# Kernel optimization log

Hardware: AMD Instinct MI355X
Metric: run time of the kernel (lower is better)

Reference implementation:

```python
import math
import jax, jax.numpy as jnp
import numpy as np

B, N, F, FE = 16, 24, 128, 128   # crystals, atoms/crystal, atom feat, edge feat
NUM_Z = 100                       # num_atomic_numbers
GAUSS_STOP, BASIS_W = 6.0, 1.0
RADIUS_RATE = 1.0
N_CONV, N_FC, FC_F = 3, 4, 128
REP = 1                           # PBC replication per axis (27 images); exact for our cells
ZDIM = 2 * F + FE


def setup_inputs() -> dict:
    key = jax.random.key(0)
    ks = jax.random.split(key, 12)
    # cubic cells with side length in [8, 10) Angstrom -> rep per axis is exactly 1
    L = 8.0 + 2.0 * jax.random.uniform(ks[0], (B,))
    cell = L[:, None, None] * jnp.eye(3, dtype=jnp.float32)          # [B,3,3]
    frac = jax.random.uniform(ks[1], (B, N, 3))
    pos = jnp.einsum('bnd,bde->bne', frac, cell).reshape(B * N, 3)   # [B*N,3]
    atomic_numbers = jax.random.randint(ks[2], (B * N,), 1, NUM_Z + 1)
    batch = jnp.repeat(jnp.arange(B), N)
    emb = jax.random.normal(ks[3], (NUM_Z, F)) * 0.1                 # embedding table
    s = 1.0 / math.sqrt(ZDIM)
    conv_Wf = jax.random.normal(ks[4], (N_CONV, ZDIM, F)) * s
    conv_bf = jnp.zeros((N_CONV, F))
    conv_Ws = jax.random.normal(ks[5], (N_CONV, ZDIM, F)) * s
    conv_bs = jnp.zeros((N_CONV, F))
    sf = 1.0 / math.sqrt(FC_F)
    fc_W = jax.random.normal(ks[6], (N_FC - 1, FC_F, FC_F)) * sf
    fc_b = jnp.zeros((N_FC - 1, FC_F))
    W_out = jax.random.normal(ks[7], (FC_F, 1)) * sf
    b_out = jnp.zeros((1,))
    return {'pos': pos, 'cell': cell, 'emb': emb,
            'conv_Wf': conv_Wf, 'conv_bf': conv_bf,
            'conv_Ws': conv_Ws, 'conv_bs': conv_bs,
            'fc_W': fc_W, 'fc_b': fc_b, 'W_out': W_out, 'b_out': b_out,
            'atomic_numbers': atomic_numbers, 'batch': batch}


def _spectral_normalize(W, iters=5, eps=1e-12):
    # power iteration; sigma differentiable through W only (u,v detached) as in torch
    u = jnp.ones((W.shape[1],), W.dtype)
    u = u / jnp.linalg.norm(u)
    for _ in range(iters):
        v = W @ u
        v = v / (jnp.linalg.norm(v) + eps)
        u = W.T @ v
        u = u / (jnp.linalg.norm(u) + eps)
    u = jax.lax.stop_gradient(u)
    v = jax.lax.stop_gradient(v)
    sigma = v @ (W @ u)
    return W / sigma


def _forward(pos, cell, emb, conv_Wf, conv_bf, conv_Ws, conv_bs,
             fc_W, fc_b, W_out, b_out, atomic_numbers):
    # ---- graph construction (PBC all-pairs, fixed 27 images, masked) ----
    r = jnp.arange(-REP, REP + 1, dtype=cell.dtype)
    grid = jnp.stack(jnp.meshgrid(r, r, r, indexing='ij'), -1).reshape(-1, 3)  # [27,3]
    pbc = jnp.einsum('cd,bde->bce', grid, cell)                                # [B,27,3]
    posb = pos.reshape(B, N, 3)
    # disp[b,i,j,c] = pos_i - (pos_j + offset_c)
    disp = posb[:, :, None, None, :] - (posb[:, None, :, None, :] + pbc[:, None, None, :, :])
    dsqr = jnp.sum(disp * disp, -1)                                            # [B,N,N,27]
    cross = jnp.cross(cell[:, 1], cell[:, 2])
    vol = jnp.sum(cell[:, 0] * cross, -1)
    radius = RADIUS_RATE * (jnp.abs(vol) / N) ** (1.0 / 3.0)                   # [B]
    rb = radius[:, None, None, None]
    mask = (dsqr <= rb * rb) & (dsqr > 1e-4)
    dist = jnp.sqrt(jnp.maximum(dsqr, 1e-12))
    mf = mask.astype(pos.dtype)
    edge_w = (jnp.cos(dist * math.pi / rb) + 1.0) * mf                         # [B,N,N,27]
    # GaussianSmearing
    goff = jnp.linspace(0.0, GAUSS_STOP, FE)
    coeff = -0.5 / (BASIS_W * (goff[1] - goff[0])) ** 2
    edge_attr = jnp.exp(coeff * (dist[..., None] - goff) ** 2)                 # [B,N,N,27,FE]

    # ---- node features ----
    feat = jnp.tanh(emb[atomic_numbers - 1]).reshape(B, N, F)

    # ---- continuous graph convs (CGCNN-style gated conv, edge_weight scaled) ----
    for l in range(N_CONV):
        Wf, Ws = conv_Wf[l], conv_Ws[l]
        gi = feat @ Wf[:F]; gj = feat @ Wf[F:2 * F]
        ge = jnp.einsum('bijce,ef->bijcf', edge_attr, Wf[2 * F:])
        g = jax.nn.sigmoid(gi[:, :, None, None, :] + gj[:, None, :, None, :] + ge + conv_bf[l])
        si = feat @ Ws[:F]; sj = feat @ Ws[F:2 * F]
        se = jnp.einsum('bijce,ef->bijcf', edge_attr, Ws[2 * F:])
        sc = jax.nn.softplus(si[:, :, None, None, :] + sj[:, None, :, None, :] + se + conv_bs[l])
        msg = g * sc * edge_w[..., None]                                       # [B,N,N,27,F]
        feat = jax.nn.softplus(feat + msg.sum((2, 3)))                         # aggregate at i

    # ---- global mean pool + spectral-norm MLP head ----
    h = feat.mean(1)                                                           # [B,F]
    for l in range(N_FC - 1):
        h = jax.nn.softplus(h @ _spectral_normalize(fc_W[l]) + fc_b[l])
    return h @ W_out + b_out                                                   # [B,1]


def reference(pos, cell, emb, conv_Wf, conv_bf, conv_Ws, conv_bs,
              fc_W, fc_b, W_out, b_out, atomic_numbers, batch):
    return _forward(pos, cell, emb, conv_Wf, conv_bf, conv_Ws, conv_bs,
                    fc_W, fc_b, W_out, b_out, atomic_numbers)
```

## Files before the change

### kernel.cpp

```cpp
#include <hip/hip_runtime.h>
#include <math.h>

#define NB 16
#define NN 24
#define NA 384
#define FF 128
#define CC 27
#define MAXNBR 32
#define MAXE 24
#define NT 20

__device__ float g_sigma[4];
__device__ float g_projA[NA*4*FF];
__device__ float g_projB[NA*4*FF];
__device__ float g_feat [NA*FF];
__device__ __align__(128) int g_flag[NA][32];
__device__ __align__(128) int g_sigdone[32];
__device__ __align__(128) int g_batchdone[32];

__device__ __forceinline__ float softplusf(float x){ return fmaxf(x,0.f) + log1pf(expf(-fabsf(x))); }
__device__ __forceinline__ float sigmoidf(float x){ return 1.f/(1.f+expf(-x)); }
__device__ __forceinline__ void st_agent(float* p, float v){
  __hip_atomic_store(p, v, __ATOMIC_RELAXED, __HIP_MEMORY_SCOPE_AGENT);
}
__device__ __forceinline__ float ld_agent(const float* p){
  return __hip_atomic_load(p, __ATOMIC_RELAXED, __HIP_MEMORY_SCOPE_AGENT);
}
__device__ __forceinline__ void st_agent_i(int* p, int v){
  __hip_atomic_store(p, v, __ATOMIC_RELAXED, __HIP_MEMORY_SCOPE_AGENT);
}
__device__ __forceinline__ int ld_agent_i(const int* p){
  return __hip_atomic_load(p, __ATOMIC_RELAXED, __HIP_MEMORY_SCOPE_AGENT);
}

__device__ __forceinline__ void band_dot2(const float* __restrict__ ga, int kmin,
                                          const float* __restrict__ Wf2,
                                          const float* __restrict__ Ws2, int f,
                                          float& ge, float& se)
{
  float g = 0.f, s = 0.f;
  #pragma unroll
  for (int t = 0; t < NT; t++) {
    float a = ga[t];
    int k = kmin + t;
    g += a * Wf2[k*FF+f];
    s += a * Ws2[k*FF+f];
  }
  ge = g; se = s;
}

__device__ __forceinline__ float gemv_q(const float* __restrict__ Wf,
                                        const float* __restrict__ Ws,
                                        const float* s_ft, int q, int f)
{
  const float* W = (q==0) ? Wf : (q==1) ? (Wf + FF*FF) : (q==2) ? Ws : (Ws + FF*FF);
  float s = 0.f;
  #pragma unroll 16
  for (int k = 0; k < FF; k++) s += s_ft[k]*W[k*FF+f];
  return s;
}

__device__ __forceinline__ void flag_set(int i, int v)
{
  asm volatile("s_waitcnt vmcnt(0)" ::: "memory");
  __syncthreads();
  if (threadIdx.x == 0) st_agent_i(&g_flag[i][0], v);
}

__device__ __forceinline__ void wait_nbrs(int n, const int* s_nj, int target)
{
  if (threadIdx.x < 64) {
    int jg = (threadIdx.x < n) ? s_nj[threadIdx.x] : -1;
    bool sat = (jg < 0);
    int guard = 0;
    for (;;) {
      if (!sat) sat = (ld_agent_i(&g_flag[jg][0]) >= target);
      if (__all(sat)) break;
      __builtin_amdgcn_s_sleep(4);
      if (++guard > (1<<18)) break;
    }
  }
  __syncthreads();
}

__global__ void __launch_bounds__(512, 4)
k_fused(const float* __restrict__ pos, const float* __restrict__ cell,
        const float* __restrict__ emb,
        const float* __restrict__ conv_Wf, const float* __restrict__ conv_bf,
        const float* __restrict__ conv_Ws, const float* __restrict__ conv_bs,
        const float* __restrict__ fc_W,  const float* __restrict__ fc_b,
        const float* __restrict__ W_out, const float* __restrict__ b_out,
        const int* __restrict__ z, float* __restrict__ out)
{
  const int tid = threadIdx.x;
  const int q = tid >> 7, f = tid & 127;

  __shared__ float s_ft[FF];
  __shared__ float s_cell[9];
  __shared__ float s_rb;
  __shared__ int   s_cnt;
  __shared__ int   s_nj[MAXNBR];
  __shared__ float s_nd[MAXNBR];
  __shared__ float s_nw[MAXNBR];
  __shared__ float s_ga[MAXE][NT];
  __shared__ int   s_km[MAXE];
  __shared__ float s_ge[MAXE][FF];
  __shared__ float s_se[MAXE][FF];
  __shared__ float s_p[4][FF];
  __shared__ float sm[4][FF];
  __shared__ float s_hh[FF], s_tmp[FF], s_red[FF];

  if (blockIdx.x < 3) {
    const int m = blockIdx.x;
    const float* W = fc_W + m*FF*FF;
    if (tid < FF) s_hh[tid] = 0.08838834764831845f;
    __syncthreads();
    for (int it = 0; it < 5; it++) {
      { float p = 0.f;
        #pragma unroll
        for (int k = q*32; k < q*32+32; k++) p += W[f*FF+k]*s_hh[k];
        sm[q][f] = p; }
      __syncthreads();
      if (tid < FF) { float s = sm[0][f]+sm[1][f]+sm[2][f]+sm[3][f];
                      s_tmp[f] = s; s_red[f] = s*s; }
      __syncthreads();
      for (int st=64; st>0; st>>=1){ if (tid<st) s_red[tid]+=s_red[tid+st]; __syncthreads(); }
      float nv = sqrtf(s_red[0]) + 1e-12f;
      __syncthreads();
      if (tid < FF) s_tmp[f] /= nv;
      __syncthreads();
      { float p = 0.f;
        #pragma unroll
        for (int r = q*32; r < q*32+32; r++) p += W[r*FF+f]*s_tmp[r];
        sm[q][f] = p; }
      __syncthreads();
      if (tid < FF) { float s = sm[0][f]+sm[1][f]+sm[2][f]+sm[3][f];
                      s_hh[f] = s; s_red[f] = s*s; }
      __syncthreads();
      for (int st=64; st>0; st>>=1){ if (tid<st) s_red[tid]+=s_red[tid+st]; __syncthreads(); }
      float nu = sqrtf(s_red[0]) + 1e-12f;
      __syncthreads();
      if (tid < FF) s_hh[f] /= nu;
      __syncthreads();
    }
    { float p = 0.f;
      #pragma unroll
      for (int k = q*32; k < q*32+32; k++) p += W[f*FF+k]*s_hh[k];
      sm[q][f] = p; }
    __syncthreads();
    if (tid < FF) s_red[f] = s_tmp[f]*(sm[0][f]+sm[1][f]+sm[2][f]+sm[3][f]);
    __syncthreads();
    for (int st=64; st>0; st>>=1){ if (tid<st) s_red[tid]+=s_red[tid+st]; __syncthreads(); }
    if (tid == 0) {
      st_agent(&g_sigma[m], s_red[0]);
      asm volatile("s_waitcnt vmcnt(0)" ::: "memory");
      __hip_atomic_fetch_add(&g_sigdone[0], 1, __ATOMIC_RELAXED, __HIP_MEMORY_SCOPE_AGENT);
    }
    return;
  }

  const int i = (int)blockIdx.x - 3;
  const int b = i / NN;

  if (tid < FF) {
    int zi = z[i]; if (zi < 1) zi = 1; if (zi > 100) zi = 100;
    s_ft[tid] = tanhf(emb[(zi-1)*FF+tid]);
  }
  if (tid >= 256 && tid < 265) s_cell[tid-256] = cell[b*9 + tid - 256];
  if (tid == 500) s_cnt = 0;
  __syncthreads();
  if (tid == 0) {
    const float* c = s_cell;
    float cx = c[4]*c[8] - c[5]*c[7];
    float cy = c[5]*c[6] - c[3]*c[8];
    float cz = c[3]*c[7] - c[4]*c[6];
    float vol = c[0]*cx + c[1]*cy + c[2]*cz;
    s_rb = cbrtf(fabsf(vol)/(float)NN);
  }
  __syncthreads();
  {
    const float rb = s_rb, rb2 = rb*rb;
    const float pix = pos[i*3+0], piy = pos[i*3+1], piz = pos[i*3+2];
    const float PI = 3.14159265358979323846f;
    for (int cand = tid; cand < NN*CC; cand += 512) {
      int j = cand / CC, c = cand - j*CC;
      float gx = (float)(c/9) - 1.0f;
      float gy = (float)((c/3)%3) - 1.0f;
      float gz = (float)(c%3) - 1.0f;
      float ox = gx*s_cell[0] + gy*s_cell[3] + gz*s_cell[6];
      float oy = gx*s_cell[1] + gy*s_cell[4] + gz*s_cell[7];
      float oz = gx*s_cell[2] + gy*s_cell[5] + gz*s_cell[8];
      int jg = b*NN + j;
      float dx = pix - (pos[jg*3+0] + ox);
      float dy = piy - (pos[jg*3+1] + oy);
      float dz = piz - (pos[jg*3+2] + oz);
      float d2 = dx*dx + dy*dy + dz*dz;
      if (d2 <= rb2 && d2 > 1e-4f) {
        float dist = sqrtf(fmaxf(d2, 1e-4f));
        float w = cosf(dist*PI/rb) + 1.0f;
        int slot = atomicAdd(&s_cnt, 1);
        if (slot < MAXNBR) { s_nj[slot] = jg; s_nd[slot] = dist; s_nw[slot] = w; }
      }
    }
  }
  __syncthreads();
  const int n0 = (s_cnt > MAXNBR) ? MAXNBR : s_cnt;
  const int n  = (n0 > MAXE) ? MAXE : n0;

  for (int idx = tid; idx < n*NT; idx += 512) {
    int e = idx / NT, t = idx - e*NT;
    float dist = s_nd[e];
    const float step  = 6.0f/127.0f;
    const float coeff = -0.5f/(step*step);
    int kmin = (int)ceilf(dist/step - 9.0f);
    kmin = kmin < 0 ? 0 : (kmin > 108 ? 108 : kmin);
    if (t == 0) s_km[e] = kmin;
    int k = kmin + t;
    float dd = dist - step*(float)k;
    s_ga[e][t] = expf(coeff*dd*dd);
  }
  __syncthreads();

  { float s0 = gemv_q(conv_Wf, conv_Ws, s_ft, q, f);
    s_p[q][f] = s0;
    st_agent(&g_projA[(i*4+q)*FF+f], s0); }
  flag_set(i, 1);

  for (int l = 0; l < 3; ++l) {
    const float* projSrc = (l==1) ? g_projB : g_projA;
    const float* Wf2 = conv_Wf + l*3*FF*FF + 2*FF*FF;
    const float* Ws2 = conv_Ws + l*3*FF*FF + 2*FF*FF;
    for (int idx = tid; idx < n*FF; idx += 512) {
      int e = idx >> 7, ff = idx & 127;
      float ge, se;
      band_dot2(&s_ga[e][0], s_km[e], Wf2, Ws2, ff, ge, se);
      s_ge[e][ff] = ge; s_se[e][ff] = se;
    }
    __syncthreads();
    wait_nbrs(n, s_nj, l+1);
    {
      const float gi = s_p[0][f], si = s_p[2][f];
      const float bff = conv_bf[l*FF+f], bsf = conv_bs[l*FF+f];
      float gjv[6], sjv[6];
      #pragma unroll
      for (int t = 0; t < 6; ++t) {
        int e = q + 4*t;
        int jg = (e < n) ? s_nj[e] : 0;
        gjv[t] = ld_agent(&projSrc[(jg*4+1)*FF+f]);
        sjv[t] = ld_agent(&projSrc[(jg*4+3)*FF+f]);
      }
      float msg = 0.f;
      #pragma unroll
      for (int t = 0; t < 6; ++t) {
        int e = q + 4*t;
        if (e < n)
          msg += sigmoidf(gi + gjv[t] + s_ge[e][f] + bff)
               * softplusf(si + sjv[t] + s_se[e][f] + bsf) * s_nw[e];
      }
      sm[q][f] = msg;
    }
    __syncthreads();
    if (tid < FF) {
      s_ft[tid] = softplusf(s_ft[tid] + sm[0][tid] + sm[1][tid]
                                      + sm[2][tid] + sm[3][tid]);
    }
    __syncthreads();
    if (l < 2) {
      const float* WfN = conv_Wf + (l+1)*3*FF*FF;
      const float* WsN = conv_Ws + (l+1)*3*FF*FF;
      float* projDst = (l==0) ? g_projB : g_projA;
      float s1 = gemv_q(WfN, WsN, s_ft, q, f);
      s_p[q][f] = s1;
      st_agent(&projDst[(i*4+q)*FF+f], s1);
      flag_set(i, l+2);
    }
  }

  if (tid < FF) st_agent(&g_feat[i*FF+tid], s_ft[tid]);
  flag_set(i, 4);
  if (i != b*NN) return;

  if (tid < 64) {
    int jg = (tid < NN) ? (b*NN + tid) : -1;
    bool sat = (jg < 0);
    int guard = 0;
    for (;;) {
      if (!sat) sat = (ld_agent_i(&g_flag[jg][0]) >= 4);
      if (__all(sat)) break;
      __builtin_amdgcn_s_sleep(4);
      if (++guard > (1<<18)) break;
    }
  }
  __syncthreads();
  if (tid < NN) st_agent_i(&g_flag[b*NN+tid][0], 0);
  if (tid == 0) {
    int guard = 0;
    while (__hip_atomic_load(&g_sigdone[0], __ATOMIC_RELAXED, __HIP_MEMORY_SCOPE_AGENT) < 3) {
      __builtin_amdgcn_s_sleep(4);
      if (++guard > (1<<18)) break;
    }
  }
  __syncthreads();
  if (tid < FF) {
    float s0 = 0.f;
    for (int a = 0; a < NN; a++) s0 += ld_agent(&g_feat[(b*NN+a)*FF+tid]);
    s_hh[tid] = s0/(float)NN;
  }
  __syncthreads();
  for (int l = 0; l < 3; l++) {
    { float p = 0.f;
      #pragma unroll
      for (int k = q*32; k < q*32+32; k++) p += s_hh[k]*fc_W[l*FF*FF + k*FF + f];
      sm[q][f] = p; }
    __syncthreads();
    if (tid < FF) {
      float s = sm[0][tid]+sm[1][tid]+sm[2][tid]+sm[3][tid];
      s_tmp[tid] = softplusf(s/ld_agent(&g_sigma[l]) + fc_b[l*FF+tid]);
    }
    __syncthreads();
    if (tid < FF) s_hh[tid] = s_tmp[tid];
    __syncthreads();
  }
  if (tid < FF) s_red[tid] = s_hh[tid]*W_out[tid];
  __syncthreads();
  if (tid < 64) {
    float t = s_red[tid] + s_red[tid+64];
    #pragma unroll
    for (int off = 32; off > 0; off >>= 1) t += __shfl_xor(t, off);
    if (tid == 0) {
      out[b] = t + b_out[0];
      int d = __hip_atomic_fetch_add(&g_batchdone[0], 1, __ATOMIC_RELAXED,
                                     __HIP_MEMORY_SCOPE_AGENT);
      if (d == NB-1) {
        __hip_atomic_store(&g_batchdone[0], 0, __ATOMIC_RELAXED, __HIP_MEMORY_SCOPE_AGENT);
        __hip_atomic_store(&g_sigdone[0],   0, __ATOMIC_RELAXED, __HIP_MEMORY_SCOPE_AGENT);
      }
    }
  }
}

extern "C" void kernel_launch(void* const* d_in, const int* in_sizes, int n_in,
                              void* d_out, int out_size, void* d_ws, size_t ws_size,
                              hipStream_t stream) {
  const float* pos     = (const float*)d_in[0];
  const float* cell    = (const float*)d_in[1];
  const float* emb     = (const float*)d_in[2];
  const float* conv_Wf = (const float*)d_in[3];
  const float* conv_bf = (const float*)d_in[4];
  const float* conv_Ws = (const float*)d_in[5];
  const float* conv_bs = (const float*)d_in[6];
  const float* fc_W    = (const float*)d_in[7];
  const float* fc_b    = (const float*)d_in[8];
  const float* W_out   = (const float*)d_in[9];
  const float* b_out   = (const float*)d_in[10];
  const int*   z       = (const int*)d_in[11];

  k_fused<<<NA+3, 512, 0, stream>>>(pos, cell, emb, conv_Wf, conv_bf,
                                    conv_Ws, conv_bs, fc_W, fc_b,
                                    W_out, b_out, z, (float*)d_out);
}
```

Measured before the change: 127.6 us.

## Process two atoms per 1024-thread block and hoist first projection before neighbor search

The fused kernel now assigns two atoms to each block of 1024 threads, giving 192+3 blocks instead of 387 blocks of 512. The idea is to halve the number of spin-waiting blocks and flag-synchronisation points. Shared buffers are duplicated per atom and neighbour waits cover both atoms' lists. The first-layer projection GEMV and its flag publication now run before the neighbour search, so neighbours can proceed earlier. The cost is a larger shared-memory footprint (s_ge/s_se are padded to 34 rows), fewer resident blocks, and each block waiting on the union of both atoms' neighbours.

```diff
diff --git a/kernel.cpp b/kernel.cpp
--- a/kernel.cpp
+++ b/kernel.cpp
@@ -8,7 +8,9 @@
 #define CC 27
 #define MAXNBR 32
 #define MAXE 24
+#define MAXEP 34
 #define NT 20
+#define NBLK (NA/2)
 
 __device__ float g_sigma[4];
 __device__ float g_projA[NA*4*FF];
@@ -60,17 +62,24 @@
   return s;
 }
 
-__device__ __forceinline__ void flag_set(int i, int v)
+__device__ __forceinline__ void flag_set2(int i0, int v)
 {
   asm volatile("s_waitcnt vmcnt(0)" ::: "memory");
   __syncthreads();
-  if (threadIdx.x == 0) st_agent_i(&g_flag[i][0], v);
-}
-
-__device__ __forceinline__ void wait_nbrs(int n, const int* s_nj, int target)
+  if (threadIdx.x == 0) {
+    st_agent_i(&g_flag[i0  ][0], v);
+    st_agent_i(&g_flag[i0+1][0], v);
+  }
+}
+
+__device__ __forceinline__ void wait_nbrs2(int n0, int n1,
+                                           const int (*s_nj)[MAXNBR], int target)
 {
   if (threadIdx.x < 64) {
-    int jg = (threadIdx.x < n) ? s_nj[threadIdx.x] : -1;
+    int lane = threadIdx.x;
+    int jg = -1;
+    if (lane < 32) { if (lane < n0)      jg = s_nj[0][lane]; }
+    else           { if (lane - 32 < n1) jg = s_nj[1][lane-32]; }
     bool sat = (jg < 0);
     int guard = 0;
     for (;;) {
@@ -83,7 +92,7 @@
   __syncthreads();
 }
 
-__global__ void __launch_bounds__(512, 4)
+__global__ void __launch_bounds__(1024, 4)
 k_fused(const float* __restrict__ pos, const float* __restrict__ cell,
         const float* __restrict__ emb,
         const float* __restrict__ conv_Wf, const float* __restrict__ conv_bf,
@@ -93,35 +102,35 @@
         const int* __restrict__ z, float* __restrict__ out)
 {
   const int tid = threadIdx.x;
-  const int q = tid >> 7, f = tid & 127;
-
-  __shared__ float s_ft[FF];
+
+  __shared__ float s_ft[2][FF];
   __shared__ float s_cell[9];
   __shared__ float s_rb;
-  __shared__ int   s_cnt;
-  __shared__ int   s_nj[MAXNBR];
-  __shared__ float s_nd[MAXNBR];
-  __shared__ float s_nw[MAXNBR];
-  __shared__ float s_ga[MAXE][NT];
-  __shared__ int   s_km[MAXE];
-  __shared__ float s_ge[MAXE][FF];
-  __shared__ float s_se[MAXE][FF];
-  __shared__ float s_p[4][FF];
-  __shared__ float sm[4][FF];
+  __shared__ int   s_cnt[2];
+  __shared__ int   s_nj[2][MAXNBR];
+  __shared__ float s_nd[2][MAXNBR];
+  __shared__ float s_nw[2][MAXNBR];
+  __shared__ float s_ga[2][MAXE][NT];
+  __shared__ int   s_km[2][MAXE];
+  __shared__ float s_ge[2][MAXEP][FF];
+  __shared__ float s_se[2][MAXEP][FF];
+  __shared__ float s_p[2][4][FF];
+  __shared__ float sm[2][4][FF];
   __shared__ float s_hh[FF], s_tmp[FF], s_red[FF];
 
-  if (blockIdx.x < 3) {
-    const int m = blockIdx.x;
+  if (blockIdx.x >= NBLK) {
+    const int m = blockIdx.x - NBLK;
+    const int q = (tid >> 7) & 3, f = tid & 127;
     const float* W = fc_W + m*FF*FF;
     if (tid < FF) s_hh[tid] = 0.08838834764831845f;
     __syncthreads();
     for (int it = 0; it < 5; it++) {
-      { float p = 0.f;
+      if (tid < 512) { float p = 0.f;
         #pragma unroll
         for (int k = q*32; k < q*32+32; k++) p += W[f*FF+k]*s_hh[k];
-        sm[q][f] = p; }
-      __syncthreads();
-      if (tid < FF) { float s = sm[0][f]+sm[1][f]+sm[2][f]+sm[3][f];
+        sm[0][q][f] = p; }
+      __syncthreads();
+      if (tid < FF) { float s = sm[0][0][f]+sm[0][1][f]+sm[0][2][f]+sm[0][3][f];
                       s_tmp[f] = s; s_red[f] = s*s; }
       __syncthreads();
       for (int st=64; st>0; st>>=1){ if (tid<st) s_red[tid]+=s_red[tid+st]; __syncthreads(); }
@@ -129,12 +138,12 @@
       __syncthreads();
       if (tid < FF) s_tmp[f] /= nv;
       __syncthreads();
-      { float p = 0.f;
+      if (tid < 512) { float p = 0.f;
         #pragma unroll
         for (int r = q*32; r < q*32+32; r++) p += W[r*FF+f]*s_tmp[r];
-        sm[q][f] = p; }
-      __syncthreads();
-      if (tid < FF) { float s = sm[0][f]+sm[1][f]+sm[2][f]+sm[3][f];
+        sm[0][q][f] = p; }
+      __syncthreads();
+      if (tid < FF) { float s = sm[0][0][f]+sm[0][1][f]+sm[0][2][f]+sm[0][3][f];
                       s_hh[f] = s; s_red[f] = s*s; }
       __syncthreads();
       for (int st=64; st>0; st>>=1){ if (tid<st) s_red[tid]+=s_red[tid+st]; __syncthreads(); }
@@ -143,12 +152,12 @@
       if (tid < FF) s_hh[f] /= nu;
       __syncthreads();
     }
-    { float p = 0.f;
+    if (tid < 512) { float p = 0.f;
       #pragma unroll
       for (int k = q*32; k < q*32+32; k++) p += W[f*FF+k]*s_hh[k];
-      sm[q][f] = p; }
-    __syncthreads();
-    if (tid < FF) s_red[f] = s_tmp[f]*(sm[0][f]+sm[1][f]+sm[2][f]+sm[3][f]);
+      sm[0][q][f] = p; }
+    __syncthreads();
+    if (tid < FF) s_red[f] = s_tmp[f]*(sm[0][0][f]+sm[0][1][f]+sm[0][2][f]+sm[0][3][f]);
     __syncthreads();
     for (int st=64; st>0; st>>=1){ if (tid<st) s_red[tid]+=s_red[tid+st]; __syncthreads(); }
     if (tid == 0) {
@@ -159,16 +168,26 @@
     return;
   }
 
-  const int i = (int)blockIdx.x - 3;
-  const int b = i / NN;
-
-  if (tid < FF) {
-    int zi = z[i]; if (zi < 1) zi = 1; if (zi > 100) zi = 100;
-    s_ft[tid] = tanhf(emb[(zi-1)*FF+tid]);
-  }
-  if (tid >= 256 && tid < 265) s_cell[tid-256] = cell[b*9 + tid - 256];
-  if (tid == 500) s_cnt = 0;
-  __syncthreads();
+  const int i0 = 2*(int)blockIdx.x;
+  const int b  = i0 / NN;
+  const int a  = tid >> 9;
+  const int ta = tid & 511;
+  const int q  = (tid >> 7) & 3;
+  const int f  = tid & 127;
+  const int i  = i0 + a;
+
+  if (tid < 2*FF) {
+    int aa = tid >> 7, ff = tid & 127;
+    int zi = z[i0 + aa]; if (zi < 1) zi = 1; if (zi > 100) zi = 100;
+    s_ft[aa][ff] = tanhf(emb[(zi-1)*FF+ff]);
+  }
+  if (tid >= 512 && tid < 521) s_cell[tid-512] = cell[b*9 + tid - 512];
+  if (tid == 1000) { s_cnt[0] = 0; s_cnt[1] = 0; }
+  __syncthreads();
+
+  { float s0 = gemv_q(conv_Wf, conv_Ws, s_ft[a], q, f);
+    s_p[a][q][f] = s0;
+    st_agent(&g_projA[(i*4+q)*FF+f], s0); }
   if (tid == 0) {
     const float* c = s_cell;
     float cx = c[4]*c[8] - c[5]*c[7];
@@ -177,12 +196,13 @@
     float vol = c[0]*cx + c[1]*cy + c[2]*cz;
     s_rb = cbrtf(fabsf(vol)/(float)NN);
   }
-  __syncthreads();
+  flag_set2(i0, 1);
+
   {
     const float rb = s_rb, rb2 = rb*rb;
     const float pix = pos[i*3+0], piy = pos[i*3+1], piz = pos[i*3+2];
     const float PI = 3.14159265358979323846f;
-    for (int cand = tid; cand < NN*CC; cand += 512) {
+    for (int cand = ta; cand < NN*CC; cand += 512) {
       int j = cand / CC, c = cand - j*CC;
       float gx = (float)(c/9) - 1.0f;
       float gy = (float)((c/3)%3) - 1.0f;
@@ -198,54 +218,50 @@
       if (d2 <= rb2 && d2 > 1e-4f) {
         float dist = sqrtf(fmaxf(d2, 1e-4f));
         float w = cosf(dist*PI/rb) + 1.0f;
-        int slot = atomicAdd(&s_cnt, 1);
-        if (slot < MAXNBR) { s_nj[slot] = jg; s_nd[slot] = dist; s_nw[slot] = w; }
+        int slot = atomicAdd(&s_cnt[a], 1);
+        if (slot < MAXNBR) { s_nj[a][slot] = jg; s_nd[a][slot] = dist; s_nw[a][slot] = w; }
       }
     }
   }
   __syncthreads();
-  const int n0 = (s_cnt > MAXNBR) ? MAXNBR : s_cnt;
-  const int n  = (n0 > MAXE) ? MAXE : n0;
-
-  for (int idx = tid; idx < n*NT; idx += 512) {
+  const int nA = (s_cnt[a] > MAXE) ? MAXE : s_cnt[a];
+  const int n0 = (s_cnt[0] > MAXE) ? MAXE : s_cnt[0];
+  const int n1 = (s_cnt[1] > MAXE) ? MAXE : s_cnt[1];
+
+  for (int idx = ta; idx < nA*NT; idx += 512) {
     int e = idx / NT, t = idx - e*NT;
-    float dist = s_nd[e];
+    float dist = s_nd[a][e];
     const float step  = 6.0f/127.0f;
     const float coeff = -0.5f/(step*step);
     int kmin = (int)ceilf(dist/step - 9.0f);
     kmin = kmin < 0 ? 0 : (kmin > 108 ? 108 : kmin);
-    if (t == 0) s_km[e] = kmin;
+    if (t == 0) s_km[a][e] = kmin;
     int k = kmin + t;
     float dd = dist - step*(float)k;
-    s_ga[e][t] = expf(coeff*dd*dd);
-  }
-  __syncthreads();
-
-  { float s0 = gemv_q(conv_Wf, conv_Ws, s_ft, q, f);
-    s_p[q][f] = s0;
-    st_agent(&g_projA[(i*4+q)*FF+f], s0); }
-  flag_set(i, 1);
+    s_ga[a][e][t] = expf(coeff*dd*dd);
+  }
+  __syncthreads();
 
   for (int l = 0; l < 3; ++l) {
     const float* projSrc = (l==1) ? g_projB : g_projA;
     const float* Wf2 = conv_Wf + l*3*FF*FF + 2*FF*FF;
     const float* Ws2 = conv_Ws + l*3*FF*FF + 2*FF*FF;
-    for (int idx = tid; idx < n*FF; idx += 512) {
+    for (int idx = ta; idx < nA*FF; idx += 512) {
       int e = idx >> 7, ff = idx & 127;
       float ge, se;
-      band_dot2(&s_ga[e][0], s_km[e], Wf2, Ws2, ff, ge, se);
-      s_ge[e][ff] = ge; s_se[e][ff] = se;
-    }
-    __syncthreads();
-    wait_nbrs(n, s_nj, l+1);
+      band_dot2(&s_ga[a][e][0], s_km[a][e], Wf2, Ws2, ff, ge, se);
+      s_ge[a][e][ff] = ge; s_se[a][e][ff] = se;
+    }
+    __syncthreads();
+    wait_nbrs2(n0, n1, s_nj, l+1);
     {
-      const float gi = s_p[0][f], si = s_p[2][f];
+      const float gi = s_p[a][0][f], si = s_p[a][2][f];
       const float bff = conv_bf[l*FF+f], bsf = conv_bs[l*FF+f];
       float gjv[6], sjv[6];
       #pragma unroll
       for (int t = 0; t < 6; ++t) {
         int e = q + 4*t;
-        int jg = (e < n) ? s_nj[e] : 0;
+        int jg = (e < nA) ? s_nj[a][e] : 0;
         gjv[t] = ld_agent(&projSrc[(jg*4+1)*FF+f]);
         sjv[t] = ld_agent(&projSrc[(jg*4+3)*FF+f]);
       }
@@ -253,32 +269,36 @@
       #pragma unroll
       for (int t = 0; t < 6; ++t) {
         int e = q + 4*t;
-        if (e < n)
-          msg += sigmoidf(gi + gjv[t] + s_ge[e][f] + bff)
-               * softplusf(si + sjv[t] + s_se[e][f] + bsf) * s_nw[e];
+        if (e < nA)
+          msg += sigmoidf(gi + gjv[t] + s_ge[a][e][f] + bff)
+               * softplusf(si + sjv[t] + s_se[a][e][f] + bsf) * s_nw[a][e];
       }
-      sm[q][f] = msg;
-    }
-    __syncthreads();
-    if (tid < FF) {
-      s_ft[tid] = softplusf(s_ft[tid] + sm[0][tid] + sm[1][tid]
-                                      + sm[2][tid] + sm[3][tid]);
+      sm[a][q][f] = msg;
+    }
+    __syncthreads();
+    if (tid < 2*FF) {
+      int aa = tid >> 7, ff = tid & 127;
+      s_ft[aa][ff] = softplusf(s_ft[aa][ff] + sm[aa][0][ff] + sm[aa][1][ff]
+                                            + sm[aa][2][ff] + sm[aa][3][ff]);
     }
     __syncthreads();
     if (l < 2) {
       const float* WfN = conv_Wf + (l+1)*3*FF*FF;
       const float* WsN = conv_Ws + (l+1)*3*FF*FF;
       float* projDst = (l==0) ? g_projB : g_projA;
-      float s1 = gemv_q(WfN, WsN, s_ft, q, f);
-      s_p[q][f] = s1;
+      float s1 = gemv_q(WfN, WsN, s_ft[a], q, f);
+      s_p[a][q][f] = s1;
       st_agent(&projDst[(i*4+q)*FF+f], s1);
-      flag_set(i, l+2);
-    }
-  }
-
-  if (tid < FF) st_agent(&g_feat[i*FF+tid], s_ft[tid]);
-  flag_set(i, 4);
-  if (i != b*NN) return;
+      flag_set2(i0, l+2);
+    }
+  }
+
+  if (tid < 2*FF) {
+    int aa = tid >> 7, ff = tid & 127;
+    st_agent(&g_feat[(i0+aa)*FF+ff], s_ft[aa][ff]);
+  }
+  flag_set2(i0, 4);
+  if (i0 != b*NN) return;
 
   if (tid < 64) {
     int jg = (tid < NN) ? (b*NN + tid) : -1;
@@ -303,18 +323,18 @@
   __syncthreads();
   if (tid < FF) {
     float s0 = 0.f;
-    for (int a = 0; a < NN; a++) s0 += ld_agent(&g_feat[(b*NN+a)*FF+tid]);
+    for (int aa = 0; aa < NN; aa++) s0 += ld_agent(&g_feat[(b*NN+aa)*FF+tid]);
     s_hh[tid] = s0/(float)NN;
   }
   __syncthreads();
   for (int l = 0; l < 3; l++) {
-    { float p = 0.f;
+    if (tid < 512) { float p = 0.f;
       #pragma unroll
       for (int k = q*32; k < q*32+32; k++) p += s_hh[k]*fc_W[l*FF*FF + k*FF + f];
-      sm[q][f] = p; }
+      sm[0][q][f] = p; }
     __syncthreads();
     if (tid < FF) {
-      float s = sm[0][tid]+sm[1][tid]+sm[2][tid]+sm[3][tid];
+      float s = sm[0][0][tid]+sm[0][1][tid]+sm[0][2][tid]+sm[0][3][tid];
       s_tmp[tid] = softplusf(s/ld_agent(&g_sigma[l]) + fc_b[l*FF+tid]);
     }
     __syncthreads();
@@ -355,7 +375,7 @@
   const float* b_out   = (const float*)d_in[10];
   const int*   z       = (const int*)d_in[11];
 
-  k_fused<<<NA+3, 512, 0, stream>>>(pos, cell, emb, conv_Wf, conv_bf,
-                                    conv_Ws, conv_bs, fc_W, fc_b,
-                                    W_out, b_out, z, (float*)d_out);
-}
+  k_fused<<<NBLK+3, 1024, 0, stream>>>(pos, cell, emb, conv_Wf, conv_bf,
+                                       conv_Ws, conv_bs, fc_W, fc_b,
+                                       W_out, b_out, z, (float*)d_out);
+}
```

New measurement: 139.0 us. 8.9% more time.

## Compute layer-0 neighbor projections locally to remove first cross-block wait

Applied to the files above, without the earlier changes.

For the first convolution layer, each block recomputes its neighbors' embedding features (tanh of the embedding row) and their j-side gate and filter projections in shared memory, instead of waiting for other blocks to publish them to global memory. This removes one inter-block flag wait and one global handoff round, and shifts flag numbering down by one. In exchange each block does up to 24 extra 128x128 GEMVs per weight matrix and uses considerably more shared memory, which may reduce occupancy.

```diff
diff --git a/kernel.cpp b/kernel.cpp
--- a/kernel.cpp
+++ b/kernel.cpp
@@ -102,6 +102,10 @@
   __shared__ int   s_nj[MAXNBR];
   __shared__ float s_nd[MAXNBR];
   __shared__ float s_nw[MAXNBR];
+  __shared__ int   s_zj[MAXE];
+  __shared__ float s_fn[MAXE][FF];
+  __shared__ float s_gj[MAXE][FF];
+  __shared__ float s_sj[MAXE][FF];
   __shared__ float s_ga[MAXE][NT];
   __shared__ int   s_km[MAXE];
   __shared__ float s_ge[MAXE][FF];
@@ -204,9 +208,11 @@
     }
   }
   __syncthreads();
-  const int n0 = (s_cnt > MAXNBR) ? MAXNBR : s_cnt;
-  const int n  = (n0 > MAXE) ? MAXE : n0;
-
+  const int n0c = (s_cnt > MAXNBR) ? MAXNBR : s_cnt;
+  const int n   = (n0c > MAXE) ? MAXE : n0c;
+
+  if (tid < n) { int zj = z[s_nj[tid]]; if (zj < 1) zj = 1; if (zj > 100) zj = 100;
+                 s_zj[tid] = zj; }
   for (int idx = tid; idx < n*NT; idx += 512) {
     int e = idx / NT, t = idx - e*NT;
     float dist = s_nd[e];
@@ -221,13 +227,62 @@
   }
   __syncthreads();
 
+  for (int idx = tid; idx < n*FF; idx += 512) {
+    int e = idx >> 7, k = idx & 127;
+    s_fn[e][k] = tanhf(emb[(s_zj[e]-1)*FF+k]);
+  }
   { float s0 = gemv_q(conv_Wf, conv_Ws, s_ft, q, f);
-    s_p[q][f] = s0;
-    st_agent(&g_projA[(i*4+q)*FF+f], s0); }
+    s_p[q][f] = s0; }
+  __syncthreads();
+  {
+    const float* WfJ = conv_Wf + FF*FF;
+    const float* WsJ = conv_Ws + FF*FF;
+    for (int idx = tid; idx < 2*n*FF; idx += 512) {
+      int e = idx >> 8, h = (idx >> 7) & 1, ff = idx & 127;
+      const float* W = (h == 0) ? WfJ : WsJ;
+      float s = 0.f;
+      #pragma unroll 16
+      for (int k = 0; k < FF; k++) s += s_fn[e][k]*W[k*FF+ff];
+      if (h == 0) s_gj[e][ff] = s; else s_sj[e][ff] = s;
+    }
+  }
+  {
+    const float* Wf2 = conv_Wf + 2*FF*FF;
+    const float* Ws2 = conv_Ws + 2*FF*FF;
+    for (int idx = tid; idx < n*FF; idx += 512) {
+      int e = idx >> 7, ff = idx & 127;
+      float ge, se;
+      band_dot2(&s_ga[e][0], s_km[e], Wf2, Ws2, ff, ge, se);
+      s_ge[e][ff] = ge; s_se[e][ff] = se;
+    }
+  }
+  __syncthreads();
+  {
+    const float gi = s_p[0][f], si = s_p[2][f];
+    const float bff = conv_bf[0*FF+f], bsf = conv_bs[0*FF+f];
+    float msg = 0.f;
+    #pragma unroll
+    for (int t = 0; t < 6; ++t) {
+      int e = q + 4*t;
+      if (e < n)
+        msg += sigmoidf(gi + s_gj[e][f] + s_ge[e][f] + bff)
+             * softplusf(si + s_sj[e][f] + s_se[e][f] + bsf) * s_nw[e];
+    }
+    sm[q][f] = msg;
+  }
+  __syncthreads();
+  if (tid < FF) {
+    s_ft[tid] = softplusf(s_ft[tid] + sm[0][tid] + sm[1][tid]
+                                    + sm[2][tid] + sm[3][tid]);
+  }
+  __syncthreads();
+  { float s1 = gemv_q(conv_Wf + 3*FF*FF, conv_Ws + 3*FF*FF, s_ft, q, f);
+    s_p[q][f] = s1;
+    st_agent(&g_projA[(i*4+q)*FF+f], s1); }
   flag_set(i, 1);
 
-  for (int l = 0; l < 3; ++l) {
-    const float* projSrc = (l==1) ? g_projB : g_projA;
+  for (int l = 1; l < 3; ++l) {
+    const float* projSrc = (l==1) ? g_projA : g_projB;
     const float* Wf2 = conv_Wf + l*3*FF*FF + 2*FF*FF;
     const float* Ws2 = conv_Ws + l*3*FF*FF + 2*FF*FF;
     for (int idx = tid; idx < n*FF; idx += 512) {
@@ -237,7 +292,7 @@
       s_ge[e][ff] = ge; s_se[e][ff] = se;
     }
     __syncthreads();
-    wait_nbrs(n, s_nj, l+1);
+    wait_nbrs(n, s_nj, l);
     {
       const float gi = s_p[0][f], si = s_p[2][f];
       const float bff = conv_bf[l*FF+f], bsf = conv_bs[l*FF+f];
@@ -265,19 +320,16 @@
                                       + sm[2][tid] + sm[3][tid]);
     }
     __syncthreads();
-    if (l < 2) {
-      const float* WfN = conv_Wf + (l+1)*3*FF*FF;
-      const float* WsN = conv_Ws + (l+1)*3*FF*FF;
-      float* projDst = (l==0) ? g_projB : g_projA;
-      float s1 = gemv_q(WfN, WsN, s_ft, q, f);
-      s_p[q][f] = s1;
-      st_agent(&projDst[(i*4+q)*FF+f], s1);
-      flag_set(i, l+2);
+    if (l == 1) {
+      float s2 = gemv_q(conv_Wf + 2*3*FF*FF, conv_Ws + 2*3*FF*FF, s_ft, q, f);
+      s_p[q][f] = s2;
+      st_agent(&g_projB[(i*4+q)*FF+f], s2);
+      flag_set(i, 2);
     }
   }
 
   if (tid < FF) st_agent(&g_feat[i*FF+tid], s_ft[tid]);
-  flag_set(i, 4);
+  flag_set(i, 3);
   if (i != b*NN) return;
 
   if (tid < 64) {
@@ -285,7 +337,7 @@
     bool sat = (jg < 0);
     int guard = 0;
     for (;;) {
-      if (!sat) sat = (ld_agent_i(&g_flag[jg][0]) >= 4);
+      if (!sat) sat = (ld_agent_i(&g_flag[jg][0]) >= 3);
       if (__all(sat)) break;
       __builtin_amdgcn_s_sleep(4);
       if (++guard > (1<<18)) break;
```

Measured after the change: 141.3 us. 10.8% more time.
